# Performance work log

Measured on AMD Instinct MI355X. Metric: run time of the kernel, lower is better.

## Reference

```python
import jax, jax.numpy as jnp
import numpy as np

NUM_LEAVES = 256
EPS = 1e-6
SHARPNESS = 1.0   # init_sharpness, non-trainable buffer
BIAS_SHIFT = -2.0


def _generalized_gcd(w1, w2, lambd):
    # lambd: per-node bias -> andness via sigmoid; broadcast over batch
    lam = jax.nn.sigmoid(lambd)
    a = jnp.abs(w1) + EPS
    b = jnp.abs(w2) + EPS
    return lam * jnp.minimum(a, b) + (1.0 - lam) * jnp.maximum(a, b)


def setup_inputs() -> dict:
    key = jax.random.key(0)
    ks = jax.random.split(key, 6)
    B, L = 65536, NUM_LEAVES
    x = jax.random.normal(ks[0], (B, L), jnp.float32)
    # xavier-like scale for the leaf projection
    W_leaf = jax.random.normal(ks[1], (L, L), jnp.float32) * (1.0 / np.sqrt(L))
    weights = jax.random.uniform(ks[2], (L - 1, 2), jnp.float32, 0.5, 1.5)
    biases = jax.random.uniform(ks[3], (L - 1,), jnp.float32) * 0.1
    w_out = jax.random.normal(ks[4], (1, 1), jnp.float32)
    b_out = jnp.full((1,), 0.5, jnp.float32)
    return {"x": x, "W_leaf": W_leaf, "weights": weights,
            "biases": biases, "w_out": w_out, "b_out": b_out}


def reference(x, W_leaf, weights, biases, w_out, b_out):
    # InputToLeafFC: sigmoid(sharpness * (x @ W^T + bias_shift))
    leaf = jax.nn.sigmoid(SHARPNESS * (x @ W_leaf.T + BIAS_SHIFT))  # (B, L)

    # The original pops two nodes from the front of the queue and appends the
    # result; for a power-of-two leaf count this is exactly a level-by-level
    # pairwise tree reduction, with node weights consumed in order.
    cur = leaf
    off = 0
    n = cur.shape[1]
    while n > 1:  # log2(L) levels, each fully vectorized over (batch, pairs)
        m = n // 2
        w = weights[off:off + m]   # (m, 2)
        b = biases[off:off + m]    # (m,)
        left = cur[:, 0::2] * w[:, 0]
        right = cur[:, 1::2] * w[:, 1]
        cur = _generalized_gcd(left, right, b)  # (B, m)
        off += m
        n = m
    # fc_out: Linear(1,1) then sigmoid -> (B, 1)
    return jax.nn.sigmoid(cur * w_out[0, 0] + b_out[0])
```

## Files before the change

### kernel.cpp

```cpp
#include <hip/hip_runtime.h>
#include <stdint.h>


#define EPS 1e-6f
#define LOG2E 1.44269504088896340736f

typedef __attribute__((ext_vector_type(8))) short short8;
typedef __attribute__((ext_vector_type(4))) short short4_t;
typedef __attribute__((ext_vector_type(4))) float float4_t;

__device__ __forceinline__ float fast_sigmoid(float z) {
    float e = __builtin_amdgcn_exp2f(-z * LOG2E);
    return __builtin_amdgcn_rcpf(1.0f + e);
}

__device__ __forceinline__ short f2bf(float f) {
    uint32_t u = __builtin_bit_cast(uint32_t, f);
    u += 0x7FFFu + ((u >> 16) & 1u);
    return (short)(u >> 16);
}

__device__ __forceinline__ short8 pack8(float4 a, float4 b) {
    short8 s;
    s[0] = f2bf(a.x); s[1] = f2bf(a.y); s[2] = f2bf(a.z); s[3] = f2bf(a.w);
    s[4] = f2bf(b.x); s[5] = f2bf(b.y); s[6] = f2bf(b.z); s[7] = f2bf(b.w);
    return s;
}

__device__ __forceinline__ float ggcd(float l, float r, float lam) {
    float a = fabsf(l) + EPS;
    float b = fabsf(r) + EPS;
    float mn = fminf(a, b);
    float mx = fmaxf(a, b);
    return fmaf(lam, mn - mx, mx);
}

__device__ __forceinline__ void tree_reduce(float4_t acc[16], int c0,
                                            const float4* pv, float res[4]) {
    #pragma unroll
    for (int t = 0; t < 16; ++t) {
        #pragma unroll
        for (int r = 0; r < 4; ++r) acc[t][r] = fast_sigmoid(acc[t][r] - 2.0f);
    }
    #pragma unroll
    for (int tp = 0; tp < 8; ++tp) {
        float4 p = pv[c0 * 8 + tp];
        #pragma unroll
        for (int r = 0; r < 4; ++r)
            acc[tp][r] = ggcd(acc[2*tp][r] * p.x, acc[2*tp+1][r] * p.y, p.z);
    }
    #pragma unroll
    for (int tp = 0; tp < 4; ++tp) {
        float4 p = pv[128 + c0 * 4 + tp];
        #pragma unroll
        for (int r = 0; r < 4; ++r)
            acc[tp][r] = ggcd(acc[2*tp][r] * p.x, acc[2*tp+1][r] * p.y, p.z);
    }
    #pragma unroll
    for (int tp = 0; tp < 2; ++tp) {
        float4 p = pv[192 + c0 * 2 + tp];
        #pragma unroll
        for (int r = 0; r < 4; ++r)
            acc[tp][r] = ggcd(acc[2*tp][r] * p.x, acc[2*tp+1][r] * p.y, p.z);
    }
    {
        float4 p = pv[224 + c0];
        #pragma unroll
        for (int r = 0; r < 4; ++r)
            res[r] = ggcd(acc[0][r] * p.x, acc[1][r] * p.y, p.z);
    }
}

__global__ __launch_bounds__(1024, 4)
void btln_main(const float* __restrict__ x, const float* __restrict__ Wl,
               const float* __restrict__ wts, const float* __restrict__ bia,
               const float* __restrict__ wout, const float* __restrict__ bout,
               float* __restrict__ out) {
    __shared__ short Wt[4][16384];
    __shared__ float4 pv[256];

    const int tid  = threadIdx.x;
    const int lane = tid & 63;
    const int wv   = tid >> 6;
    const int c0   = lane & 15;
    const int q    = lane >> 4;

    if (tid < 255) {
        pv[tid] = make_float4(wts[2 * tid], wts[2 * tid + 1],
                              fast_sigmoid(bia[tid]), 0.f);
    } else if (tid == 255) {
        pv[255] = make_float4(0.f, 0.f, 0.f, 0.f);
    }

    {
        const int scpos = tid & 7;
        const int sj    = (tid >> 3) & 63;
        const int half  = tid >> 9;
        const int jA    = sj + 128 * half;
        const int jB    = jA + 64;
        const int colx  = (scpos ^ (sj & 7)) << 3;
        const int srcA  = ((jA & 15) << 4) | (jA >> 4);
        const int srcB  = ((jB & 15) << 4) | (jB >> 4);
        #pragma unroll
        for (int kt = 0; kt < 4; ++kt) {
            const float* pA = Wl + srcA * 256 + kt * 64 + colx;
            const float* pB = Wl + srcB * 256 + kt * 64 + colx;
            float4 a0 = *(const float4*)(pA);
            float4 a1 = *(const float4*)(pA + 4);
            float4 b0 = *(const float4*)(pB);
            float4 b1 = *(const float4*)(pB + 4);
            char* base = (char*)&Wt[kt][0] + scpos * 16;
            *(short8*)(base + jA * 128) = pack8(a0, a1);
            *(short8*)(base + jB * 128) = pack8(b0, b1);
        }
    }

    const int rowbase = blockIdx.x * 256 + wv * 16;
    const float* xr = x + (size_t)(rowbase + c0) * 256;

    float4 r0 = *(const float4*)(xr + q * 8);
    float4 r1 = *(const float4*)(xr + q * 8 + 4);
    float4 r2 = *(const float4*)(xr + 32 + q * 8);
    float4 r3 = *(const float4*)(xr + 32 + q * 8 + 4);
    short8 afc0 = pack8(r0, r1);
    short8 afc1 = pack8(r2, r3);

    float4_t acc[16];
    #pragma unroll
    for (int t = 0; t < 16; ++t) acc[t] = (float4_t){0.f, 0.f, 0.f, 0.f};

    __syncthreads();

    const int vx = c0 & 7;

#define MFMA_T(t)                                                             \
    {                                                                         \
        const short* base = &cur[((t) * 16 + c0) * 64];                       \
        short8 bf0 = *(const short8*)&base[(q ^ vx) * 8];                     \
        short8 bf1 = *(const short8*)&base[((q + 4) ^ vx) * 8];               \
        acc[t] = __builtin_amdgcn_mfma_f32_16x16x32_bf16(                     \
            afc0, bf0, acc[t], 0, 0, 0);                                      \
        acc[t] = __builtin_amdgcn_mfma_f32_16x16x32_bf16(                     \
            afc1, bf1, acc[t], 0, 0, 0);                                      \
    }

#define KSTEP(kt, LAST)                                                       \
    {                                                                         \
        const short* cur = &Wt[kt][0];                                        \
        float4 n0, n1, n2, n3;                                                \
        if (!(LAST)) {                          \
            const float* xn = xr + ((kt) + 1) * 64;                           \
            n0 = *(const float4*)(xn + q * 8);                                \
            n1 = *(const float4*)(xn + q * 8 + 4);                            \
            n2 = *(const float4*)(xn + 32 + q * 8);                           \
            n3 = *(const float4*)(xn + 32 + q * 8 + 4);                       \
        }                                                                     \
        _Pragma("unroll")                                                     \
        for (int t = 0; t < 16; ++t) MFMA_T(t)                                \
        if (!(LAST)) {                                                        \
            afc0 = pack8(n0, n1);                                             \
            afc1 = pack8(n2, n3);                                             \
        }                                                                     \
        __builtin_amdgcn_sched_barrier(0);       \
    }

    KSTEP(0, 0)
    KSTEP(1, 0)
    KSTEP(2, 0)
    KSTEP(3, 1)
#undef KSTEP
#undef MFMA_T

    float res[4];
    tree_reduce(acc, c0, pv, res);

    const int offs[4] = {240, 248, 252, 254};
    #pragma unroll
    for (int k = 0; k < 4; ++k) {
        float4 p = pv[offs[k] + (c0 >> (k + 1))];
        bool isLeft = ((c0 >> k) & 1) == 0;
        #pragma unroll
        for (int r = 0; r < 4; ++r) {
            float other = __shfl_xor(res[r], 1 << k, 64);
            float lf = isLeft ? res[r] : other;
            float rt = isLeft ? other  : res[r];
            res[r] = ggcd(lf * p.x, rt * p.y, p.z);
        }
    }

    if (c0 == 0) {
        const float wo = wout[0];
        const float bo = bout[0];
        #pragma unroll
        for (int r = 0; r < 4; ++r)
            out[rowbase + q * 4 + r] = fast_sigmoid(fmaf(res[r], wo, bo));
    }
}

extern "C" void kernel_launch(void* const* d_in, const int* in_sizes, int n_in,
                              void* d_out, int out_size, void* d_ws, size_t ws_size,
                              hipStream_t stream) {
    const float* x   = (const float*)d_in[0];
    const float* Wl  = (const float*)d_in[1];
    const float* wts = (const float*)d_in[2];
    const float* bia = (const float*)d_in[3];
    const float* wo  = (const float*)d_in[4];
    const float* bo  = (const float*)d_in[5];
    float* out = (float*)d_out;

    const int rows = out_size;
    dim3 grid(rows / 256), block(1024);
    btln_main<<<grid, block, 0, stream>>>(x, Wl, wts, bia, wo, bo, out);
}
```

Baseline: 114.6 us.

## Process two 16-row tiles per wave to reuse LDS weight fragments

Each wave now computes two 16-row M tiles, loading each B fragment from shared memory once and feeding it to two MFMA chains. The block shrinks to 512 threads covering the same 256 rows, and the weight staging loop is rewritten so each thread packs four rows. This aims to cut LDS read traffic per MFMA, but doubles accumulator registers and halves the threads per block available for weight staging and latency hiding.

```diff
diff --git a/kernel.cpp b/kernel.cpp
--- a/kernel.cpp
+++ b/kernel.cpp
@@ -71,7 +71,30 @@
     }
 }
 
-__global__ __launch_bounds__(1024, 4)
+__device__ __forceinline__ void tree_tail(float res[4], int c0, int q,
+                                          const float4* pv, float wo, float bo,
+                                          float* __restrict__ out, int rb) {
+    const int offs[4] = {240, 248, 252, 254};
+    #pragma unroll
+    for (int k = 0; k < 4; ++k) {
+        float4 p = pv[offs[k] + (c0 >> (k + 1))];
+        bool isLeft = ((c0 >> k) & 1) == 0;
+        #pragma unroll
+        for (int r = 0; r < 4; ++r) {
+            float other = __shfl_xor(res[r], 1 << k, 64);
+            float lf = isLeft ? res[r] : other;
+            float rt = isLeft ? other  : res[r];
+            res[r] = ggcd(lf * p.x, rt * p.y, p.z);
+        }
+    }
+    if (c0 == 0) {
+        #pragma unroll
+        for (int r = 0; r < 4; ++r)
+            out[rb + q * 4 + r] = fast_sigmoid(fmaf(res[r], wo, bo));
+    }
+}
+
+__global__ __launch_bounds__(512, 2)
 void btln_main(const float* __restrict__ x, const float* __restrict__ Wl,
                const float* __restrict__ wts, const float* __restrict__ bia,
                const float* __restrict__ wout, const float* __restrict__ bout,
@@ -94,40 +117,45 @@
 
     {
         const int scpos = tid & 7;
-        const int sj    = (tid >> 3) & 63;
-        const int half  = tid >> 9;
-        const int jA    = sj + 128 * half;
-        const int jB    = jA + 64;
+        const int sj    = tid >> 3;
         const int colx  = (scpos ^ (sj & 7)) << 3;
-        const int srcA  = ((jA & 15) << 4) | (jA >> 4);
-        const int srcB  = ((jB & 15) << 4) | (jB >> 4);
-        #pragma unroll
-        for (int kt = 0; kt < 4; ++kt) {
-            const float* pA = Wl + srcA * 256 + kt * 64 + colx;
-            const float* pB = Wl + srcB * 256 + kt * 64 + colx;
-            float4 a0 = *(const float4*)(pA);
-            float4 a1 = *(const float4*)(pA + 4);
-            float4 b0 = *(const float4*)(pB);
-            float4 b1 = *(const float4*)(pB + 4);
-            char* base = (char*)&Wt[kt][0] + scpos * 16;
-            *(short8*)(base + jA * 128) = pack8(a0, a1);
-            *(short8*)(base + jB * 128) = pack8(b0, b1);
+        #pragma unroll
+        for (int half = 0; half < 4; ++half) {
+            const int j   = sj + 64 * half;
+            const int src = ((j & 15) << 4) | (j >> 4);
+            #pragma unroll
+            for (int kt = 0; kt < 4; ++kt) {
+                const float* p = Wl + src * 256 + kt * 64 + colx;
+                float4 a0 = *(const float4*)(p);
+                float4 a1 = *(const float4*)(p + 4);
+                *(short8*)((char*)&Wt[kt][0] + j * 128 + scpos * 16) = pack8(a0, a1);
+            }
         }
     }
 
-    const int rowbase = blockIdx.x * 256 + wv * 16;
-    const float* xr = x + (size_t)(rowbase + c0) * 256;
-
-    float4 r0 = *(const float4*)(xr + q * 8);
-    float4 r1 = *(const float4*)(xr + q * 8 + 4);
-    float4 r2 = *(const float4*)(xr + 32 + q * 8);
-    float4 r3 = *(const float4*)(xr + 32 + q * 8 + 4);
-    short8 afc0 = pack8(r0, r1);
-    short8 afc1 = pack8(r2, r3);
-
-    float4_t acc[16];
-    #pragma unroll
-    for (int t = 0; t < 16; ++t) acc[t] = (float4_t){0.f, 0.f, 0.f, 0.f};
+    const int rowbase = blockIdx.x * 256 + wv * 32;
+    const float* xrA = x + (size_t)(rowbase + c0) * 256;
+    const float* xrB = x + (size_t)(rowbase + 16 + c0) * 256;
+
+    float4 r0 = *(const float4*)(xrA + q * 8);
+    float4 r1 = *(const float4*)(xrA + q * 8 + 4);
+    float4 r2 = *(const float4*)(xrA + 32 + q * 8);
+    float4 r3 = *(const float4*)(xrA + 32 + q * 8 + 4);
+    float4 s0 = *(const float4*)(xrB + q * 8);
+    float4 s1 = *(const float4*)(xrB + q * 8 + 4);
+    float4 s2 = *(const float4*)(xrB + 32 + q * 8);
+    float4 s3 = *(const float4*)(xrB + 32 + q * 8 + 4);
+    short8 afA0 = pack8(r0, r1);
+    short8 afA1 = pack8(r2, r3);
+    short8 afB0 = pack8(s0, s1);
+    short8 afB1 = pack8(s2, s3);
+
+    float4_t accA[16], accB[16];
+    #pragma unroll
+    for (int t = 0; t < 16; ++t) {
+        accA[t] = (float4_t){0.f, 0.f, 0.f, 0.f};
+        accB[t] = (float4_t){0.f, 0.f, 0.f, 0.f};
+    }
 
     __syncthreads();
 
@@ -138,28 +166,39 @@
         const short* base = &cur[((t) * 16 + c0) * 64];                       \
         short8 bf0 = *(const short8*)&base[(q ^ vx) * 8];                     \
         short8 bf1 = *(const short8*)&base[((q + 4) ^ vx) * 8];               \
-        acc[t] = __builtin_amdgcn_mfma_f32_16x16x32_bf16(                     \
-            afc0, bf0, acc[t], 0, 0, 0);                                      \
-        acc[t] = __builtin_amdgcn_mfma_f32_16x16x32_bf16(                     \
-            afc1, bf1, acc[t], 0, 0, 0);                                      \
+        accA[t] = __builtin_amdgcn_mfma_f32_16x16x32_bf16(                    \
+            afA0, bf0, accA[t], 0, 0, 0);                                     \
+        accA[t] = __builtin_amdgcn_mfma_f32_16x16x32_bf16(                    \
+            afA1, bf1, accA[t], 0, 0, 0);                                     \
+        accB[t] = __builtin_amdgcn_mfma_f32_16x16x32_bf16(                    \
+            afB0, bf0, accB[t], 0, 0, 0);                                     \
+        accB[t] = __builtin_amdgcn_mfma_f32_16x16x32_bf16(                    \
+            afB1, bf1, accB[t], 0, 0, 0);                                     \
     }
 
 #define KSTEP(kt, LAST)                                                       \
     {                                                                         \
         const short* cur = &Wt[kt][0];                                        \
-        float4 n0, n1, n2, n3;                                                \
+        float4 n0, n1, n2, n3, m0, m1, m2, m3;                                \
         if (!(LAST)) {                          \
-            const float* xn = xr + ((kt) + 1) * 64;                           \
-            n0 = *(const float4*)(xn + q * 8);                                \
-            n1 = *(const float4*)(xn + q * 8 + 4);                            \
-            n2 = *(const float4*)(xn + 32 + q * 8);                           \
-            n3 = *(const float4*)(xn + 32 + q * 8 + 4);                       \
+            const float* xnA = xrA + ((kt) + 1) * 64;                         \
+            const float* xnB = xrB + ((kt) + 1) * 64;                         \
+            n0 = *(const float4*)(xnA + q * 8);                               \
+            n1 = *(const float4*)(xnA + q * 8 + 4);                           \
+            n2 = *(const float4*)(xnA + 32 + q * 8);                          \
+            n3 = *(const float4*)(xnA + 32 + q * 8 + 4);                      \
+            m0 = *(const float4*)(xnB + q * 8);                               \
+            m1 = *(const float4*)(xnB + q * 8 + 4);                           \
+            m2 = *(const float4*)(xnB + 32 + q * 8);                          \
+            m3 = *(const float4*)(xnB + 32 + q * 8 + 4);                      \
         }                                                                     \
         _Pragma("unroll")                                                     \
         for (int t = 0; t < 16; ++t) MFMA_T(t)                                \
         if (!(LAST)) {                                                        \
-            afc0 = pack8(n0, n1);                                             \
-            afc1 = pack8(n2, n3);                                             \
+            afA0 = pack8(n0, n1);                                             \
+            afA1 = pack8(n2, n3);                                             \
+            afB0 = pack8(m0, m1);                                             \
+            afB1 = pack8(m2, m3);                                             \
         }                                                                     \
         __builtin_amdgcn_sched_barrier(0);       \
     }
@@ -171,29 +210,17 @@
 #undef KSTEP
 #undef MFMA_T
 
-    float res[4];
-    tree_reduce(acc, c0, pv, res);
-
-    const int offs[4] = {240, 248, 252, 254};
-    #pragma unroll
-    for (int k = 0; k < 4; ++k) {
-        float4 p = pv[offs[k] + (c0 >> (k + 1))];
-        bool isLeft = ((c0 >> k) & 1) == 0;
-        #pragma unroll
-        for (int r = 0; r < 4; ++r) {
-            float other = __shfl_xor(res[r], 1 << k, 64);
-            float lf = isLeft ? res[r] : other;
-            float rt = isLeft ? other  : res[r];
-            res[r] = ggcd(lf * p.x, rt * p.y, p.z);
-        }
-    }
-
-    if (c0 == 0) {
-        const float wo = wout[0];
-        const float bo = bout[0];
-        #pragma unroll
-        for (int r = 0; r < 4; ++r)
-            out[rowbase + q * 4 + r] = fast_sigmoid(fmaf(res[r], wo, bo));
+    const float wo = wout[0];
+    const float bo = bout[0];
+    {
+        float res[4];
+        tree_reduce(accA, c0, pv, res);
+        tree_tail(res, c0, q, pv, wo, bo, out, rowbase);
+    }
+    {
+        float res[4];
+        tree_reduce(accB, c0, pv, res);
+        tree_tail(res, c0, q, pv, wo, bo, out, rowbase + 16);
     }
 }
 
@@ -209,6 +236,6 @@
     float* out = (float*)d_out;
 
     const int rows = out_size;
-    dim3 grid(rows / 256), block(1024);
+    dim3 grid(rows / 256), block(512);
     btln_main<<<grid, block, 0, stream>>>(x, Wl, wts, bia, wo, bo, out);
 }
```

Measured after the change: 113.9 us. No clear change (-0.7%).
